# Performance work log

Measured on AMD Instinct MI355X. Metric: run time of the kernel, lower is better.

## Reference

```python
import jax, jax.numpy as jnp
import numpy as np

K_CODES, D_DIM = 512, 64


def setup_inputs() -> dict:
    key = jax.random.key(0)
    k1, k2 = jax.random.split(key)
    x = jax.random.normal(k1, (32, D_DIM, 64, 64), dtype=jnp.float32)  # NCHW
    weight = jax.random.uniform(k2, (K_CODES, D_DIM), minval=-1.0 / K_CODES,
                                maxval=1.0 / K_CODES, dtype=jnp.float32)
    return {"x": x, "weight": weight}


def reference(x, weight):
    K = weight.shape[0]
    xp = jnp.transpose(x, (0, 2, 3, 1))          # [B, H, W, D]
    flat = xp.reshape(-1, weight.shape[1])       # [N, D]
    dist = (jnp.sum(flat * flat, axis=1, keepdims=True)
            + jnp.sum(weight * weight, axis=1)
            - 2.0 * flat @ weight.T)
    idx = jnp.argmin(dist, axis=1)               # [N]
    enc = jax.nn.one_hot(idx, K, dtype=jnp.float32)   # [N, K] one-hot scatter
    quantized = (enc @ weight).reshape(xp.shape)      # matmul codebook lookup
    commit_loss = jnp.mean(jnp.square(jax.lax.stop_gradient(quantized) - xp))
    vq_loss = jnp.mean(jnp.square(quantized - jax.lax.stop_gradient(xp)))
    loss = vq_loss + 1.0 * commit_loss           # commitment_cost = 1.0
    quant_st = xp + jax.lax.stop_gradient(quantized - xp)  # straight-through
    return (loss, jnp.transpose(quant_st, (0, 3, 1, 2)), enc, idx)
```

## Files before the change

### kernel.cpp

```cpp
#include <hip/hip_runtime.h>
#include <cfloat>

#define KC 512
#define DD 64
#define HW 4096
#define NPIX 131072
#define QSIZE 8388608
#define PXB 128
#define NTILE (NPIX / PXB)
#define NBLK (NTILE / 2)
#define NTH 512
#define MARGIN 4.0e-3f

typedef short short8 __attribute__((ext_vector_type(8)));
typedef float f32x4 __attribute__((ext_vector_type(4)));
typedef float nfloat4 __attribute__((ext_vector_type(4)));
typedef unsigned long long u64;

__device__ __forceinline__ unsigned short bf16_rne(float f) {
    unsigned int u = __float_as_uint(f);
    u += 0x7FFFu + ((u >> 16) & 1u);
    return (unsigned short)(u >> 16);
}

__device__ __forceinline__ void barrier_lds_only() {
    asm volatile("s_waitcnt lgkmcnt(0)" ::: "memory");
    __builtin_amdgcn_s_barrier();
    __builtin_amdgcn_sched_barrier(0);
}

__global__ __launch_bounds__(1024) void prep(
    const float* __restrict__ w, float* __restrict__ w2g,
    uint4* __restrict__ wswz) {
  const int gt = blockIdx.x * 1024 + threadIdx.x;
  {
    int ct = gt >> 7, kc = (gt >> 6) & 1, ln = gt & 63;
    int n = ln & 15, q = ln >> 4;
    const float* wp = w + (ct * 16 + n) * DD + kc * 32 + q * 8;
    nfloat4 f0 = *(const nfloat4*)(wp);
    nfloat4 f1 = *(const nfloat4*)(wp + 4);
    uint4 u;
    u.x = (unsigned)bf16_rne(f0[0]) | ((unsigned)bf16_rne(f0[1]) << 16);
    u.y = (unsigned)bf16_rne(f0[2]) | ((unsigned)bf16_rne(f0[3]) << 16);
    u.z = (unsigned)bf16_rne(f1[0]) | ((unsigned)bf16_rne(f1[1]) << 16);
    u.w = (unsigned)bf16_rne(f1[2]) | ((unsigned)bf16_rne(f1[3]) << 16);
    wswz[gt] = u;
  }
  if (gt < KC) {
    const float* wk = w + gt * DD;
    float r0 = __fmul_rn(wk[0], wk[0]), r1 = __fmul_rn(wk[1], wk[1]),
          r2 = __fmul_rn(wk[2], wk[2]), r3 = __fmul_rn(wk[3], wk[3]),
          r4 = __fmul_rn(wk[4], wk[4]), r5 = __fmul_rn(wk[5], wk[5]),
          r6 = __fmul_rn(wk[6], wk[6]), r7 = __fmul_rn(wk[7], wk[7]);
    #pragma unroll
    for (int i = 8; i < DD; i += 8) {
      r0 = __fadd_rn(r0, __fmul_rn(wk[i+0], wk[i+0]));
      r1 = __fadd_rn(r1, __fmul_rn(wk[i+1], wk[i+1]));
      r2 = __fadd_rn(r2, __fmul_rn(wk[i+2], wk[i+2]));
      r3 = __fadd_rn(r3, __fmul_rn(wk[i+3], wk[i+3]));
      r4 = __fadd_rn(r4, __fmul_rn(wk[i+4], wk[i+4]));
      r5 = __fadd_rn(r5, __fmul_rn(wk[i+5], wk[i+5]));
      r6 = __fadd_rn(r6, __fmul_rn(wk[i+6], wk[i+6]));
      r7 = __fadd_rn(r7, __fmul_rn(wk[i+7], wk[i+7]));
    }
    w2g[gt] = __fadd_rn(__fadd_rn(__fadd_rn(r0, r1), __fadd_rn(r2, r3)),
                        __fadd_rn(__fadd_rn(r4, r5), __fadd_rn(r6, r7)));
  }
}


__device__ __forceinline__ void tile_prelude(
    const float* __restrict__ xt, float* Xs, u64 (*candm)[8],
    short8& a0, short8& a1, int tid, int lane, int wv) {
  ((u64*)candm)[tid] = 0;
  ((u64*)candm)[tid + NTH] = 0;
  if (tid < PXB) {
    const float* xp = xt + tid;
    float r0 = __fmul_rn(xp[0*HW], xp[0*HW]), r1 = __fmul_rn(xp[1*HW], xp[1*HW]),
          r2 = __fmul_rn(xp[2*HW], xp[2*HW]), r3 = __fmul_rn(xp[3*HW], xp[3*HW]),
          r4 = __fmul_rn(xp[4*HW], xp[4*HW]), r5 = __fmul_rn(xp[5*HW], xp[5*HW]),
          r6 = __fmul_rn(xp[6*HW], xp[6*HW]), r7 = __fmul_rn(xp[7*HW], xp[7*HW]);
    #pragma unroll
    for (int i = 8; i < DD; i += 8) {
      r0 = __fadd_rn(r0, __fmul_rn(xp[(size_t)(i+0)*HW], xp[(size_t)(i+0)*HW]));
      r1 = __fadd_rn(r1, __fmul_rn(xp[(size_t)(i+1)*HW], xp[(size_t)(i+1)*HW]));
      r2 = __fadd_rn(r2, __fmul_rn(xp[(size_t)(i+2)*HW], xp[(size_t)(i+2)*HW]));
      r3 = __fadd_rn(r3, __fmul_rn(xp[(size_t)(i+3)*HW], xp[(size_t)(i+3)*HW]));
      r4 = __fadd_rn(r4, __fmul_rn(xp[(size_t)(i+4)*HW], xp[(size_t)(i+4)*HW]));
      r5 = __fadd_rn(r5, __fmul_rn(xp[(size_t)(i+5)*HW], xp[(size_t)(i+5)*HW]));
      r6 = __fadd_rn(r6, __fmul_rn(xp[(size_t)(i+6)*HW], xp[(size_t)(i+6)*HW]));
      r7 = __fadd_rn(r7, __fmul_rn(xp[(size_t)(i+7)*HW], xp[(size_t)(i+7)*HW]));
    }
    Xs[tid] = __fadd_rn(__fadd_rn(__fadd_rn(r0, r1), __fadd_rn(r2, r3)),
                        __fadd_rn(__fadd_rn(r4, r5), __fadd_rn(r6, r7)));
  }
  const int am = lane & 15, aq = lane >> 4;
  const float* xa = xt + wv * 16 + am;
  #pragma unroll
  for (int j = 0; j < 8; ++j) {
    a0[j] = (short)bf16_rne(-2.0f * xa[(size_t)(aq * 8 + j) * HW]);
    a1[j] = (short)bf16_rne(-2.0f * xa[(size_t)(32 + aq * 8 + j) * HW]);
  }
}

__device__ __forceinline__ void tile_screen(
    const short8* wl8, const float* w2s, u64 (*candm)[8],
    short8 a0, short8 a1, int lane, int wv) {
  const int cn = lane & 15;
  float m0 = FLT_MAX, m1 = FLT_MAX, m2 = FLT_MAX, m3 = FLT_MAX;
  for (int ct = 0; ct < 32; ++ct) {
    float wk2 = w2s[ct * 16 + cn];
    f32x4 acc = {wk2, wk2, wk2, wk2};
    acc = __builtin_amdgcn_mfma_f32_16x16x32_bf16(a0, wl8[ct * 128 + lane], acc, 0, 0, 0);
    acc = __builtin_amdgcn_mfma_f32_16x16x32_bf16(a1, wl8[ct * 128 + 64 + lane], acc, 0, 0, 0);
    m0 = fminf(m0, acc[0]); m1 = fminf(m1, acc[1]);
    m2 = fminf(m2, acc[2]); m3 = fminf(m3, acc[3]);
  }
  #pragma unroll
  for (int s = 1; s < 16; s <<= 1) {
    m0 = fminf(m0, __shfl_xor(m0, s));
    m1 = fminf(m1, __shfl_xor(m1, s));
    m2 = fminf(m2, __shfl_xor(m2, s));
    m3 = fminf(m3, __shfl_xor(m3, s));
  }
  const float t0 = m0 + MARGIN, t1 = m1 + MARGIN,
              t2 = m2 + MARGIN, t3 = m3 + MARGIN;
  for (int ct = 0; ct < 32; ++ct) {
    float wk2 = w2s[ct * 16 + cn];
    f32x4 acc = {wk2, wk2, wk2, wk2};
    acc = __builtin_amdgcn_mfma_f32_16x16x32_bf16(a0, wl8[ct * 128 + lane], acc, 0, 0, 0);
    acc = __builtin_amdgcn_mfma_f32_16x16x32_bf16(a1, wl8[ct * 128 + 64 + lane], acc, 0, 0, 0);
    u64 bm0 = __ballot(acc[0] <= t0);
    u64 bm1 = __ballot(acc[1] <= t1);
    u64 bm2 = __ballot(acc[2] <= t2);
    u64 bm3 = __ballot(acc[3] <= t3);
    if (lane < 4) {
      u64 mk = (lane == 0) ? bm0 : (lane == 1) ? bm1 : (lane == 2) ? bm2 : bm3;
      int word = ct >> 2, sh = (ct & 3) * 16;
      #pragma unroll
      for (int q = 0; q < 4; ++q) {
        u64 bits = (mk >> (q * 16)) & 0xFFFFull;
        if (bits) candm[wv * 16 + q * 4 + lane][word] |= bits << sh;
      }
    }
  }
}

__device__ __forceinline__ void tile_refine(
    const float* __restrict__ xt, const float* __restrict__ w,
    const float* w2s, const float* Xs, const u64 (*candm)[8],
    int* sidx, float* __restrict__ out_idx, int bix, int tid, int lane) {
  const int px = tid >> 2, part = tid & 3;
  const float X = Xs[px];
  const float* xr = xt + px;
  float bestd = FLT_MAX; int bk = 1 << 30;
  for (int wd = part * 2; wd < part * 2 + 2; ++wd) {
    u64 msk = candm[px][wd];
    while (msk) {
      int bit = __ffsll((unsigned long long)msk) - 1;
      msk &= msk - 1;
      int k = wd * 64 + bit;
      const float* wp = w + k * DD;
      float P = 0.f;
      #pragma unroll
      for (int dc = 0; dc < 16; ++dc) {
        nfloat4 w4 = *(const nfloat4*)(wp + dc * 4);
        P = __fmaf_rn(xr[(size_t)(dc * 4 + 0) * HW], w4[0], P);
        P = __fmaf_rn(xr[(size_t)(dc * 4 + 1) * HW], w4[1], P);
        P = __fmaf_rn(xr[(size_t)(dc * 4 + 2) * HW], w4[2], P);
        P = __fmaf_rn(xr[(size_t)(dc * 4 + 3) * HW], w4[3], P);
      }
      float dist = __fsub_rn(__fadd_rn(X, w2s[k]), __fadd_rn(P, P));
      if (dist < bestd || (dist == bestd && k < bk)) { bestd = dist; bk = k; }
    }
  }
  float od = __shfl_down(bestd, 1); int ok = __shfl_down(bk, 1);
  if ((lane & 3) < 3 && (od < bestd || (od == bestd && ok < bk))) { bestd = od; bk = ok; }
  od = __shfl_down(bestd, 2); ok = __shfl_down(bk, 2);
  if ((lane & 3) < 2 && (od < bestd || (od == bestd && ok < bk))) { bestd = od; bk = ok; }
  if (part == 0) {
    sidx[px] = bk;
    out_idx[bix * PXB + px] = (float)bk;
  }
}

__device__ __forceinline__ float tile_quant(
    const float* __restrict__ xt, const float* __restrict__ w,
    const int* sidx, float* __restrict__ qb, int tid) {
  float lsum = 0.f;
  for (int i = tid; i < PXB * DD; i += NTH) {
    int d = i >> 7, pp = i & 127;
    float qv = w[sidx[pp] * DD + d];
    float dv = qv - xt[(size_t)d * HW + pp];
    lsum = __fmaf_rn(dv, dv, lsum);
    __builtin_nontemporal_store(qv, qb + (size_t)d * HW + pp);
  }
  return lsum;
}

__device__ __forceinline__ void tile_enc(
    const int* sidx, float* __restrict__ basep, int tid) {
  for (int t = tid; t < 16383; t += NTH) {
    int u = 3 + 4 * t;
    nfloat4 v;
    #pragma unroll
    for (int j = 0; j < 4; ++j) {
      int e = u + j;
      v[j] = (sidx[e >> 9] == (e & 511)) ? 1.0f : 0.0f;
    }
    __builtin_nontemporal_store(v, (nfloat4*)(basep + u));
  }
  if (tid < 3) basep[tid] = (sidx[0] == tid) ? 1.0f : 0.0f;
  else if (tid == 3) basep[PXB * KC - 1] = (sidx[127] == 511) ? 1.0f : 0.0f;
}

__global__ __launch_bounds__(NTH, 4) void vq_fused(
    const float* __restrict__ x, const float* __restrict__ w,
    const float* __restrict__ w2g, const uint4* __restrict__ wswz,
    float* __restrict__ out_q, float* __restrict__ out_enc,
    float* __restrict__ out_idx, double* __restrict__ partial) {

  __shared__ uint4 wlds[4096];
  __shared__ float w2s[KC];
  __shared__ u64 candm[PXB][8];
  __shared__ float Xs[PXB];
  __shared__ int sidx[PXB];
  __shared__ float sredf[8];

  const int tid = threadIdx.x;
  const int lane = tid & 63;
  const int wv = tid >> 6;

  const int bix0 = blockIdx.x;
  const int b0 = bix0 >> 5;
  const int q0 = (bix0 & 31) * PXB;
  const float* xt0 = x + (size_t)b0 * (DD * HW) + q0;
  const int bix1 = blockIdx.x + NBLK;
  const int b1 = bix1 >> 5;
  const int q1 = (bix1 & 31) * PXB;
  const float* xt1 = x + (size_t)b1 * (DD * HW) + q1;

  #pragma unroll
  for (int s = 0; s < 8; ++s) wlds[tid + s * NTH] = wswz[tid + s * NTH];
  w2s[tid] = w2g[tid];

  short8 a0, a1;
  tile_prelude(xt0, Xs, candm, a0, a1, tid, lane, wv);
  __syncthreads();

  const short8* wl8 = (const short8*)wlds;

  tile_screen(wl8, w2s, candm, a0, a1, lane, wv);
  barrier_lds_only();
  tile_refine(xt0, w, w2s, Xs, candm, sidx, out_idx, bix0, tid, lane);
  barrier_lds_only();

  tile_prelude(xt1, Xs, candm, a0, a1, tid, lane, wv);
  {
    float lsum = tile_quant(xt0, w, sidx, out_q + (size_t)b0 * (DD * HW) + q0, tid);
    #pragma unroll
    for (int off = 32; off > 0; off >>= 1) lsum += __shfl_down(lsum, off);
    if (lane == 0) sredf[wv] = lsum;
  }
  tile_enc(sidx, out_enc + (size_t)bix0 * (PXB * KC), tid);
  barrier_lds_only();
  if (tid == 0) {
    double t = 0.0;
    #pragma unroll
    for (int i = 0; i < 8; ++i) t += (double)sredf[i];
    partial[bix0] = t;
  }

  tile_screen(wl8, w2s, candm, a0, a1, lane, wv);
  barrier_lds_only();
  tile_refine(xt1, w, w2s, Xs, candm, sidx, out_idx, bix1, tid, lane);
  barrier_lds_only();
  {
    float lsum = tile_quant(xt1, w, sidx, out_q + (size_t)b1 * (DD * HW) + q1, tid);
    #pragma unroll
    for (int off = 32; off > 0; off >>= 1) lsum += __shfl_down(lsum, off);
    if (lane == 0) sredf[wv] = lsum;
  }
  tile_enc(sidx, out_enc + (size_t)bix1 * (PXB * KC), tid);
  barrier_lds_only();
  if (tid == 0) {
    double t = 0.0;
    #pragma unroll
    for (int i = 0; i < 8; ++i) t += (double)sredf[i];
    partial[bix1] = t;
  }
}

__global__ void finish_kernel(const double* __restrict__ partial,
                              float* __restrict__ out) {
  int t = threadIdx.x;
  double s = partial[t] + partial[t + 256] + partial[t + 512] + partial[t + 768];
  #pragma unroll
  for (int off = 32; off > 0; off >>= 1) s += __shfl_down(s, off);
  __shared__ double sr[4];
  if ((t & 63) == 0) sr[t >> 6] = s;
  __syncthreads();
  if (t == 0)
    out[0] = (float)(2.0 * (sr[0] + sr[1] + sr[2] + sr[3]) / (double)QSIZE);
}

extern "C" void kernel_launch(void* const* d_in, const int* in_sizes, int n_in,
                              void* d_out, int out_size, void* d_ws, size_t ws_size,
                              hipStream_t stream) {
  const float* x = (const float*)d_in[0];
  const float* w = (const float*)d_in[1];
  float* out = (float*)d_out;
  float* out_q = out + 1;
  float* out_enc = out_q + QSIZE;
  float* out_idx = out_enc + (size_t)NPIX * KC;

  double* partial = (double*)d_ws;
  float* w2g = (float*)((char*)d_ws + 8192);
  uint4* wswz = (uint4*)((char*)d_ws + 16384);

  prep<<<4, 1024, 0, stream>>>(w, w2g, wswz);
  vq_fused<<<NBLK, NTH, 0, stream>>>(x, w, w2g, wswz, out_q, out_enc, out_idx, partial);
  finish_kernel<<<1, 256, 0, stream>>>(partial, out);
}
```

Measured before the change: 381.2 us.

## Cache screen distances in registers and read codebook from global instead of LDS

```diff
diff --git a/kernel.cpp b/kernel.cpp
--- a/kernel.cpp
+++ b/kernel.cpp
@@ -100,49 +100,6 @@
   for (int j = 0; j < 8; ++j) {
     a0[j] = (short)bf16_rne(-2.0f * xa[(size_t)(aq * 8 + j) * HW]);
     a1[j] = (short)bf16_rne(-2.0f * xa[(size_t)(32 + aq * 8 + j) * HW]);
-  }
-}
-
-__device__ __forceinline__ void tile_screen(
-    const short8* wl8, const float* w2s, u64 (*candm)[8],
-    short8 a0, short8 a1, int lane, int wv) {
-  const int cn = lane & 15;
-  float m0 = FLT_MAX, m1 = FLT_MAX, m2 = FLT_MAX, m3 = FLT_MAX;
-  for (int ct = 0; ct < 32; ++ct) {
-    float wk2 = w2s[ct * 16 + cn];
-    f32x4 acc = {wk2, wk2, wk2, wk2};
-    acc = __builtin_amdgcn_mfma_f32_16x16x32_bf16(a0, wl8[ct * 128 + lane], acc, 0, 0, 0);
-    acc = __builtin_amdgcn_mfma_f32_16x16x32_bf16(a1, wl8[ct * 128 + 64 + lane], acc, 0, 0, 0);
-    m0 = fminf(m0, acc[0]); m1 = fminf(m1, acc[1]);
-    m2 = fminf(m2, acc[2]); m3 = fminf(m3, acc[3]);
-  }
-  #pragma unroll
-  for (int s = 1; s < 16; s <<= 1) {
-    m0 = fminf(m0, __shfl_xor(m0, s));
-    m1 = fminf(m1, __shfl_xor(m1, s));
-    m2 = fminf(m2, __shfl_xor(m2, s));
-    m3 = fminf(m3, __shfl_xor(m3, s));
-  }
-  const float t0 = m0 + MARGIN, t1 = m1 + MARGIN,
-              t2 = m2 + MARGIN, t3 = m3 + MARGIN;
-  for (int ct = 0; ct < 32; ++ct) {
-    float wk2 = w2s[ct * 16 + cn];
-    f32x4 acc = {wk2, wk2, wk2, wk2};
-    acc = __builtin_amdgcn_mfma_f32_16x16x32_bf16(a0, wl8[ct * 128 + lane], acc, 0, 0, 0);
-    acc = __builtin_amdgcn_mfma_f32_16x16x32_bf16(a1, wl8[ct * 128 + 64 + lane], acc, 0, 0, 0);
-    u64 bm0 = __ballot(acc[0] <= t0);
-    u64 bm1 = __ballot(acc[1] <= t1);
-    u64 bm2 = __ballot(acc[2] <= t2);
-    u64 bm3 = __ballot(acc[3] <= t3);
-    if (lane < 4) {
-      u64 mk = (lane == 0) ? bm0 : (lane == 1) ? bm1 : (lane == 2) ? bm2 : bm3;
-      int word = ct >> 2, sh = (ct & 3) * 16;
-      #pragma unroll
-      for (int q = 0; q < 4; ++q) {
-        u64 bits = (mk >> (q * 16)) & 0xFFFFull;
-        if (bits) candm[wv * 16 + q * 4 + lane][word] |= bits << sh;
-      }
-    }
   }
 }
 
@@ -214,13 +171,61 @@
   else if (tid == 3) basep[PXB * KC - 1] = (sidx[127] == 511) ? 1.0f : 0.0f;
 }
 
+#define SCREEN_AND_FLAG(a0_, a1_)                                              \
+  {                                                                            \
+    float m0 = FLT_MAX, m1 = FLT_MAX, m2 = FLT_MAX, m3 = FLT_MAX;              \
+    _Pragma("unroll")                                                          \
+    for (int ct = 0; ct < 32; ++ct) {                                          \
+      float wk2 = w2s[ct * 16 + cn];                                           \
+      short8 b0 = wsw8[ct * 128 + lane];                                       \
+      short8 b1 = wsw8[ct * 128 + 64 + lane];                                  \
+      f32x4 acc = {wk2, wk2, wk2, wk2};                                        \
+      acc = __builtin_amdgcn_mfma_f32_16x16x32_bf16(a0_, b0, acc, 0, 0, 0);    \
+      acc = __builtin_amdgcn_mfma_f32_16x16x32_bf16(a1_, b1, acc, 0, 0, 0);    \
+      p[2 * ct] = (__float_as_uint(acc[1]) & 0xFFFF0000u) |                    \
+                  (__float_as_uint(acc[0]) >> 16);                             \
+      p[2 * ct + 1] = (__float_as_uint(acc[3]) & 0xFFFF0000u) |                \
+                      (__float_as_uint(acc[2]) >> 16);                         \
+      m0 = fminf(m0, acc[0]); m1 = fminf(m1, acc[1]);                          \
+      m2 = fminf(m2, acc[2]); m3 = fminf(m3, acc[3]);                          \
+    }                                                                          \
+    _Pragma("unroll")                                                          \
+    for (int s = 1; s < 16; s <<= 1) {                                         \
+      m0 = fminf(m0, __shfl_xor(m0, s));                                       \
+      m1 = fminf(m1, __shfl_xor(m1, s));                                       \
+      m2 = fminf(m2, __shfl_xor(m2, s));                                       \
+      m3 = fminf(m3, __shfl_xor(m3, s));                                       \
+    }                                                                          \
+    const float t0 = m0 + MARGIN, t1 = m1 + MARGIN,                            \
+                t2 = m2 + MARGIN, t3 = m3 + MARGIN;                            \
+    _Pragma("unroll")                                                          \
+    for (int ct = 0; ct < 32; ++ct) {                                          \
+      float f0 = __uint_as_float(p[2 * ct] << 16);                             \
+      float f1 = __uint_as_float(p[2 * ct] & 0xFFFF0000u);                     \
+      float f2 = __uint_as_float(p[2 * ct + 1] << 16);                         \
+      float f3 = __uint_as_float(p[2 * ct + 1] & 0xFFFF0000u);                 \
+      u64 bm0 = __ballot(f0 <= t0);                                            \
+      u64 bm1 = __ballot(f1 <= t1);                                            \
+      u64 bm2 = __ballot(f2 <= t2);                                            \
+      u64 bm3 = __ballot(f3 <= t3);                                            \
+      if (lane < 4) {                                                          \
+        u64 mk = (lane == 0) ? bm0 : (lane == 1) ? bm1 : (lane == 2) ? bm2 : bm3; \
+        int word = ct >> 2, sh = (ct & 3) * 16;                                \
+        _Pragma("unroll")                                                      \
+        for (int q = 0; q < 4; ++q) {                                          \
+          u64 bits = (mk >> (q * 16)) & 0xFFFFull;                             \
+          if (bits) candm[wv * 16 + q * 4 + lane][word] |= bits << sh;         \
+        }                                                                      \
+      }                                                                        \
+    }                                                                          \
+  }
+
 __global__ __launch_bounds__(NTH, 4) void vq_fused(
     const float* __restrict__ x, const float* __restrict__ w,
-    const float* __restrict__ w2g, const uint4* __restrict__ wswz,
+    const float* __restrict__ w2g, const short8* __restrict__ wsw8,
     float* __restrict__ out_q, float* __restrict__ out_enc,
     float* __restrict__ out_idx, double* __restrict__ partial) {
 
-  __shared__ uint4 wlds[4096];
   __shared__ float w2s[KC];
   __shared__ u64 candm[PXB][8];
   __shared__ float Xs[PXB];
@@ -230,6 +235,7 @@
   const int tid = threadIdx.x;
   const int lane = tid & 63;
   const int wv = tid >> 6;
+  const int cn = lane & 15;
 
   const int bix0 = blockIdx.x;
   const int b0 = bix0 >> 5;
@@ -240,17 +246,14 @@
   const int q1 = (bix1 & 31) * PXB;
   const float* xt1 = x + (size_t)b1 * (DD * HW) + q1;
 
-  #pragma unroll
-  for (int s = 0; s < 8; ++s) wlds[tid + s * NTH] = wswz[tid + s * NTH];
   w2s[tid] = w2g[tid];
 
+  unsigned p[64];
   short8 a0, a1;
   tile_prelude(xt0, Xs, candm, a0, a1, tid, lane, wv);
   __syncthreads();
 
-  const short8* wl8 = (const short8*)wlds;
-
-  tile_screen(wl8, w2s, candm, a0, a1, lane, wv);
+  SCREEN_AND_FLAG(a0, a1)
   barrier_lds_only();
   tile_refine(xt0, w, w2s, Xs, candm, sidx, out_idx, bix0, tid, lane);
   barrier_lds_only();
@@ -271,7 +274,7 @@
     partial[bix0] = t;
   }
 
-  tile_screen(wl8, w2s, candm, a0, a1, lane, wv);
+  SCREEN_AND_FLAG(a0, a1)
   barrier_lds_only();
   tile_refine(xt1, w, w2s, Xs, candm, sidx, out_idx, bix1, tid, lane);
   barrier_lds_only();
@@ -319,6 +322,7 @@
   uint4* wswz = (uint4*)((char*)d_ws + 16384);
 
   prep<<<4, 1024, 0, stream>>>(w, w2g, wswz);
-  vq_fused<<<NBLK, NTH, 0, stream>>>(x, w, w2g, wswz, out_q, out_enc, out_idx, partial);
+  vq_fused<<<NBLK, NTH, 0, stream>>>(x, w, w2g, (const short8*)wswz,
+                                     out_q, out_enc, out_idx, partial);
   finish_kernel<<<1, 256, 0, stream>>>(partial, out);
 }
```

Result: slower. 494.7 us (+29.8%).
